# Performance work log

Measured on AMD Instinct MI355X. Metric: run time of the kernel, lower is better.

The kernel has to match this reference:

```python
import jax, jax.numpy as jnp
import numpy as np

B, D_IN, D_S = 16384, 1024, 1024


def setup_inputs() -> dict:
    key = jax.random.key(0)
    ks = jax.random.split(key, 7)
    s_in = 1.0 / np.sqrt(D_IN)
    s_h = 1.0 / np.sqrt(D_S)
    return {
        "input": jax.random.normal(ks[0], (B, D_IN), jnp.float32),
        "cell_state": jax.random.normal(ks[1], (B, D_S), jnp.float32),
        "hidden_state": jax.random.normal(ks[2], (B, D_S), jnp.float32),
        "Wx": jax.random.uniform(ks[3], (4, D_S, D_IN), jnp.float32, -s_in, s_in),
        "bx": jax.random.uniform(ks[4], (4, D_S), jnp.float32, -s_in, s_in),
        "Wh": jax.random.uniform(ks[5], (4, D_S, D_S), jnp.float32, -s_h, s_h),
        "bh": jax.random.uniform(ks[6], (4, D_S), jnp.float32, -s_h, s_h),
    }


def reference(input, cell_state, hidden_state, Wx, bx, Wh, bh):
    # Fused: two batched GEMMs produce all 4 gate pre-activations.
    # gates_x, gates_h: [4, B, D_S]; gate order: forget, input, cand, output
    gx = jnp.einsum('bi,gsi->gbs', input, Wx) + bx[:, None, :]
    gh = jnp.einsum('bh,gsh->gbs', hidden_state, Wh) + bh[:, None, :]
    pre = gx + gh
    f = jax.nn.sigmoid(pre[0])
    i = jax.nn.sigmoid(pre[1]) * jnp.tanh(pre[2])
    new_cell_state = cell_state * f + i
    output = jnp.tanh(new_cell_state) * jax.nn.sigmoid(pre[3])
    return (new_cell_state, output)
```

## Files before the change

### kernel.cpp

```cpp
#include <hip/hip_runtime.h>
#include <hip/hip_bf16.h>
#include <stdint.h>


typedef short bf16x8 __attribute__((ext_vector_type(8)));
typedef float f32x4 __attribute__((ext_vector_type(4)));

#define B_ROWS 16384
#define D_K 2048

__device__ __forceinline__ unsigned short f2bf(float f) {
    unsigned u = __builtin_bit_cast(unsigned, f);
    u += 0x7FFFu + ((u >> 16) & 1u);
    return (unsigned short)(u >> 16);
}

__device__ __forceinline__ float sigf(float x) { return 1.0f / (1.0f + __expf(-x)); }
__device__ __forceinline__ float tanhfast(float x) { return 2.0f / (1.0f + __expf(-2.0f * x)) - 1.0f; }

#define GLD16(gp, lp)                                                          \
    __builtin_amdgcn_global_load_lds(                                          \
        (const __attribute__((address_space(1))) unsigned int*)(gp),           \
        (__attribute__((address_space(3))) unsigned int*)(lp), 16, 0, 0)

#define FENCE() asm volatile("" ::: "memory")


__global__ void pack_A_kernel(const float* __restrict__ x,
                              const float* __restrict__ h,
                              unsigned short* __restrict__ A) {
    const int total = B_ROWS * (D_K / 4);
    for (int v = blockIdx.x * blockDim.x + threadIdx.x; v < total;
         v += gridDim.x * blockDim.x) {
        const int b = v >> 9;
        const int k0 = (v & 511) << 2;
        const float* src = (k0 < 1024) ? (x + (size_t)b * 1024 + k0)
                                       : (h + (size_t)b * 1024 + (k0 - 1024));
        float4 f = *(const float4*)src;
        unsigned p0 = (unsigned)f2bf(f.x) | ((unsigned)f2bf(f.y) << 16);
        unsigned p1 = (unsigned)f2bf(f.z) | ((unsigned)f2bf(f.w) << 16);
        uint2 o; o.x = p0; o.y = p1;
        *(uint2*)(A + (size_t)v * 4) = o;
    }
}

__global__ void pack_W_kernel(const float* __restrict__ Wx,
                              const float* __restrict__ Wh,
                              unsigned short* __restrict__ W) {
    const int total = 4096 * (D_K / 4);
    for (int v = blockIdx.x * blockDim.x + threadIdx.x; v < total;
         v += gridDim.x * blockDim.x) {
        const int n = v >> 9;
        const int k0 = (v & 511) << 2;
        const float* src = (k0 < 1024) ? (Wx + (size_t)n * 1024 + k0)
                                       : (Wh + (size_t)n * 1024 + (k0 - 1024));
        float4 f = *(const float4*)src;
        unsigned p0 = (unsigned)f2bf(f.x) | ((unsigned)f2bf(f.y) << 16);
        unsigned p1 = (unsigned)f2bf(f.z) | ((unsigned)f2bf(f.w) << 16);
        uint2 o; o.x = p0; o.y = p1;
        *(uint2*)(W + (size_t)v * 4) = o;
    }
}

__global__ void pack_bias_kernel(const float* __restrict__ bx,
                                 const float* __restrict__ bh,
                                 float* __restrict__ bias) {
    int i = blockIdx.x * blockDim.x + threadIdx.x;
    if (i < 4096) bias[i] = bx[i] + bh[i];
}


__global__ __launch_bounds__(512, 4) void lstm_gemm_kernel(
    const unsigned short* __restrict__ A,
    const unsigned short* __restrict__ W,
    const float* __restrict__ bias,
    const float* __restrict__ cell,
    float* __restrict__ out) {
    __shared__ __align__(16) unsigned short smem[2][12288];

    const int bid = blockIdx.x;
    const int wgi = (bid & 7) * 256 + (bid >> 3);
    const int brow = (wgi & 127) << 7;
    const int bcol = (wgi >> 7) << 6;

    const int tid = threadIdx.x;
    const int wid = tid >> 6;
    const int lane = tid & 63;
    const int wr = wid >> 2;
    const int wc = wid & 3;
    const int lr = lane & 15, lg = lane >> 4;
    const int l16 = lane >> 2;
    const int lk = (((lane & 3) ^ (l16 & 3)) << 3);

    f32x4 acc[4][4];
#pragma unroll
    for (int g = 0; g < 4; ++g)
#pragma unroll
        for (int m = 0; m < 4; ++m) acc[g][m] = (f32x4){0.f, 0.f, 0.f, 0.f};

    const unsigned short* gp[3];
#pragma unroll
    for (int i = 0; i < 3; ++i) {
        const int c = wid * 3 + i;
        if (c < 8) {
            gp[i] = A + (size_t)(brow + c * 16 + l16) * D_K + lk;
        } else {
            const int cw = c - 8;
            gp[i] = W + (size_t)((cw >> 2) * 1024 + bcol + (cw & 3) * 16 + l16) * D_K + lk;
        }
    }

#define STAGE(buf, kt)                                                         \
    do {                                                                       \
        char* _d = (char*)smem[buf] + (wid * 3) * 1024;                        \
        _Pragma("unroll")                                                      \
        for (int _i = 0; _i < 3; ++_i) GLD16(gp[_i] + (kt), _d + _i * 1024);   \
    } while (0)

#define COMPUTE(buf)                                                           \
    do {                                                                       \
        const unsigned short* _sb = smem[buf];                                 \
        const int _sl = ((lg ^ (lr & 3)) << 3);                                \
        bf16x8 a[4], w[4];                                                     \
        _Pragma("unroll")                                                      \
        for (int m = 0; m < 4; ++m)                                            \
            a[m] = *(const bf16x8*)&_sb[(wr * 4 + m) * 512 + lr * 32 + _sl];   \
        _Pragma("unroll")                                                      \
        for (int g = 0; g < 4; ++g)                                            \
            w[g] = *(const bf16x8*)&_sb[(8 + g * 4 + wc) * 512 + lr * 32 + _sl]; \
        __builtin_amdgcn_s_setprio(1);                                         \
        _Pragma("unroll")                                                      \
        for (int g = 0; g < 4; ++g) {                                          \
            _Pragma("unroll")                                                  \
            for (int m = 0; m < 4; ++m)                                        \
                acc[g][m] = __builtin_amdgcn_mfma_f32_16x16x32_bf16(           \
                    a[m], w[g], acc[g][m], 0, 0, 0);                           \
        }                                                                      \
        __builtin_amdgcn_s_setprio(0);                                         \
    } while (0)

    STAGE(0, 0);

    for (int t = 0; t < 63; ++t) {
        STAGE((t + 1) & 1, (t + 1) * 32);
        asm volatile("s_waitcnt vmcnt(3)" ::: "memory");
        __builtin_amdgcn_s_barrier();
        FENCE();
        COMPUTE(t & 1);
        FENCE();
        __builtin_amdgcn_s_barrier();
        FENCE();
    }
    asm volatile("s_waitcnt vmcnt(0)" ::: "memory");
    __builtin_amdgcn_s_barrier();
    FENCE();
    COMPUTE(1);

#undef STAGE
#undef COMPUTE

    float bv[4];
#pragma unroll
    for (int g = 0; g < 4; ++g) bv[g] = bias[(g << 10) + bcol + wc * 16 + lr];

    float* outc = out;
    float* outh = out + (size_t)B_ROWS * 1024;
#pragma unroll
    for (int m = 0; m < 4; ++m) {
#pragma unroll
        for (int r = 0; r < 4; ++r) {
            const int b = brow + wr * 64 + m * 16 + lg * 4 + r;
            const size_t idx = (size_t)b * 1024 + bcol + wc * 16 + lr;
            float pf = acc[0][m][r] + bv[0];
            float pi = acc[1][m][r] + bv[1];
            float pc = acc[2][m][r] + bv[2];
            float po = acc[3][m][r] + bv[3];
            float cl = cell[idx];
            float nc = cl * sigf(pf) + sigf(pi) * tanhfast(pc);
            outc[idx] = nc;
            outh[idx] = tanhfast(nc) * sigf(po);
        }
    }
}


__global__ void lstm_naive_kernel(const float* __restrict__ x,
                                  const float* __restrict__ cell,
                                  const float* __restrict__ h,
                                  const float* __restrict__ Wx,
                                  const float* __restrict__ bx,
                                  const float* __restrict__ Wh,
                                  const float* __restrict__ bh,
                                  float* __restrict__ out) {
    int idx = blockIdx.x * blockDim.x + threadIdx.x;
    if (idx >= B_ROWS * 1024) return;
    int b = idx >> 10, s = idx & 1023;
    const float* xr = x + (size_t)b * 1024;
    const float* hr = h + (size_t)b * 1024;
    float pre[4];
#pragma unroll
    for (int g = 0; g < 4; ++g) {
        float acc = bx[(g << 10) + s] + bh[(g << 10) + s];
        const float* wx = Wx + ((size_t)(g << 10) + s) * 1024;
        const float* wh = Wh + ((size_t)(g << 10) + s) * 1024;
        for (int k = 0; k < 1024; ++k) acc += xr[k] * wx[k] + hr[k] * wh[k];
        pre[g] = acc;
    }
    float nc = cell[idx] * sigf(pre[0]) + sigf(pre[1]) * tanhfast(pre[2]);
    out[idx] = nc;
    out[(size_t)B_ROWS * 1024 + idx] = tanhfast(nc) * sigf(pre[3]);
}


extern "C" void kernel_launch(void* const* d_in, const int* in_sizes, int n_in,
                              void* d_out, int out_size, void* d_ws, size_t ws_size,
                              hipStream_t stream) {
    const float* x    = (const float*)d_in[0];
    const float* cell = (const float*)d_in[1];
    const float* hid  = (const float*)d_in[2];
    const float* Wx   = (const float*)d_in[3];
    const float* bx   = (const float*)d_in[4];
    const float* Wh   = (const float*)d_in[5];
    const float* bh   = (const float*)d_in[6];
    float* out = (float*)d_out;

    const size_t szA = (size_t)B_ROWS * D_K * 2;
    const size_t szW = (size_t)4096 * D_K * 2;
    const size_t szB = 4096 * 4;
    if (ws_size < szA + szW + szB) {
        lstm_naive_kernel<<<(B_ROWS * 1024) / 256, 256, 0, stream>>>(
            x, cell, hid, Wx, bx, Wh, bh, out);
        return;
    }

    unsigned short* Ab = (unsigned short*)d_ws;
    unsigned short* Wb = (unsigned short*)((char*)d_ws + szA);
    float* bias = (float*)((char*)d_ws + szA + szW);

    pack_A_kernel<<<8192, 256, 0, stream>>>(x, hid, Ab);
    pack_W_kernel<<<2048, 256, 0, stream>>>(Wx, Wh, Wb);
    pack_bias_kernel<<<16, 256, 0, stream>>>(bx, bh, bias);

    lstm_gemm_kernel<<<2048, 512, 0, stream>>>(Ab, Wb, bias, cell, out);
}
```

Baseline: 368.3 us.

## Load weight fragments directly into registers instead of staging through LDS

Only the activation tile is staged in shared memory now, shrinking LDS from two 24KB buffers to two 8KB buffers. Each wave reads its weight MFMA operands straight from global memory into registers one k-step ahead, and the A swizzle is adjusted to match. The aim is to cut LDS traffic and footprint, which may raise occupancy. In exchange, waves sharing a column group load the same weights redundantly, the per-row global reads are narrow, and the weight-load latency is only partly hidden by one compute step.

```diff
diff --git a/kernel.cpp b/kernel.cpp
--- a/kernel.cpp
+++ b/kernel.cpp
@@ -76,7 +76,7 @@
     const float* __restrict__ bias,
     const float* __restrict__ cell,
     float* __restrict__ out) {
-    __shared__ __align__(16) unsigned short smem[2][12288];
+    __shared__ __align__(16) unsigned short smem[2][4096];
 
     const int bid = blockIdx.x;
     const int wgi = (bid & 7) * 256 + (bid >> 3);
@@ -90,7 +90,7 @@
     const int wc = wid & 3;
     const int lr = lane & 15, lg = lane >> 4;
     const int l16 = lane >> 2;
-    const int lk = (((lane & 3) ^ (l16 & 3)) << 3);
+    const int lk = (((lane & 3) ^ ((lane >> 3) & 3)) << 3);
 
     f32x4 acc[4][4];
 #pragma unroll
@@ -98,36 +98,30 @@
 #pragma unroll
         for (int m = 0; m < 4; ++m) acc[g][m] = (f32x4){0.f, 0.f, 0.f, 0.f};
 
-    const unsigned short* gp[3];
-#pragma unroll
-    for (int i = 0; i < 3; ++i) {
-        const int c = wid * 3 + i;
-        if (c < 8) {
-            gp[i] = A + (size_t)(brow + c * 16 + l16) * D_K + lk;
-        } else {
-            const int cw = c - 8;
-            gp[i] = W + (size_t)((cw >> 2) * 1024 + bcol + (cw & 3) * 16 + l16) * D_K + lk;
-        }
-    }
-
-#define STAGE(buf, kt)                                                         \
+    const unsigned short* gpA = A + (size_t)(brow + wid * 16 + l16) * D_K + lk;
+    const unsigned short* gpW[4];
+#pragma unroll
+    for (int g = 0; g < 4; ++g)
+        gpW[g] = W + (size_t)(g * 1024 + bcol + wc * 16 + lr) * D_K + lg * 8;
+
+    bf16x8 w[4];
+
+#define STAGE_A(buf, kt)  GLD16(gpA + (kt), (char*)smem[buf] + wid * 1024)
+#define LOADW(kt)                                                              \
     do {                                                                       \
-        char* _d = (char*)smem[buf] + (wid * 3) * 1024;                        \
         _Pragma("unroll")                                                      \
-        for (int _i = 0; _i < 3; ++_i) GLD16(gp[_i] + (kt), _d + _i * 1024);   \
+        for (int _g = 0; _g < 4; ++_g)                                         \
+            w[_g] = *(const bf16x8*)(gpW[_g] + (kt));                          \
     } while (0)
 
 #define COMPUTE(buf)                                                           \
     do {                                                                       \
         const unsigned short* _sb = smem[buf];                                 \
-        const int _sl = ((lg ^ (lr & 3)) << 3);                                \
-        bf16x8 a[4], w[4];                                                     \
+        const int _sl = ((lg ^ ((lr >> 1) & 3)) << 3);                         \
+        bf16x8 a[4];                                                           \
         _Pragma("unroll")                                                      \
         for (int m = 0; m < 4; ++m)                                            \
-            a[m] = *(const bf16x8*)&_sb[(wr * 4 + m) * 512 + lr * 32 + _sl];   \
-        _Pragma("unroll")                                                      \
-        for (int g = 0; g < 4; ++g)                                            \
-            w[g] = *(const bf16x8*)&_sb[(8 + g * 4 + wc) * 512 + lr * 32 + _sl]; \
+            a[m] = *(const bf16x8*)&_sb[(wr * 64 + m * 16 + lr) * 32 + _sl];   \
         __builtin_amdgcn_s_setprio(1);                                         \
         _Pragma("unroll")                                                      \
         for (int g = 0; g < 4; ++g) {                                          \
@@ -139,24 +133,34 @@
         __builtin_amdgcn_s_setprio(0);                                         \
     } while (0)
 
-    STAGE(0, 0);
-
-    for (int t = 0; t < 63; ++t) {
-        STAGE((t + 1) & 1, (t + 1) * 32);
-        asm volatile("s_waitcnt vmcnt(3)" ::: "memory");
+    LOADW(0);
+    STAGE_A(0, 0);
+    STAGE_A(1, 32);
+
+    for (int t = 0; t < 62; ++t) {
+        asm volatile("s_waitcnt vmcnt(1)" ::: "memory");
         __builtin_amdgcn_s_barrier();
         FENCE();
         COMPUTE(t & 1);
+        LOADW((t + 1) * 32);
         FENCE();
         __builtin_amdgcn_s_barrier();
         FENCE();
-    }
+        STAGE_A(t & 1, (t + 2) * 32);
+    }
+    asm volatile("s_waitcnt vmcnt(1)" ::: "memory");
+    __builtin_amdgcn_s_barrier();
+    FENCE();
+    COMPUTE(0);
+    LOADW(63 * 32);
+    FENCE();
     asm volatile("s_waitcnt vmcnt(0)" ::: "memory");
     __builtin_amdgcn_s_barrier();
     FENCE();
     COMPUTE(1);
 
-#undef STAGE
+#undef STAGE_A
+#undef LOADW
 #undef COMPUTE
 
     float bv[4];
```

Result: slower. 587.1 us (+59.4%).
